# Optimization experiments

Hardware: AMD Instinct MI355X
Metric: run time of the kernel (lower is better)

The kernel has to match this reference:

```python
import jax, jax.numpy as jnp
import numpy as np

RES = 0.03
NUM_ROTS = 36
NUM_PROPOSAL = 256
OVERSAMPLE = 4           # fixed-size stand-in for the data-dependent while loop
GX, GY, GZ = 272, 112, 272  # grid covering [-4,4.16] x [-0.2,3.16] x [-4,4.16] at res=0.03
POW = 0.5
SEED_DIST_THRESH = 0.3


def setup_inputs() -> dict:
    key = jax.random.key(0)
    ks = jax.random.split(key, 6)
    N, M = 100000, 1024
    extent = jnp.array([7.0, 3.0, 7.0], jnp.float32)
    offset = jnp.array([-3.5, 0.0, -3.5], jnp.float32)
    pc = jax.random.uniform(ks[0], (N, 3), jnp.float32) * extent + offset
    xyz = jax.random.uniform(ks[1], (N, 3), jnp.float32, minval=-0.3, maxval=0.3)
    scale = jax.random.uniform(ks[2], (N, 3), jnp.float32, minval=0.1, maxval=1.0)
    prob = jax.random.uniform(ks[3], (N,), jnp.float32)
    corners = jnp.array([[-4.0, -0.2, -4.0], [4.16, 3.16, 4.16]], jnp.float32)
    vote_points = jax.random.uniform(ks[4], (M, 3), jnp.float32) * extent + offset
    return dict(pc=pc, xyz=xyz, scale=scale, prob=prob, corners=corners, vote_points=vote_points)


def hough_vote(pc, xyz, scale, prob, corners):
    # Each point casts NUM_ROTS votes: center = pc + R_y(theta) @ xyz_offset
    thetas = 2.0 * jnp.pi * jnp.arange(NUM_ROTS, dtype=jnp.float32) / NUM_ROTS
    c, s = jnp.cos(thetas), jnp.sin(thetas)  # [R]
    ox, oy, oz = xyz[:, 0:1], xyz[:, 1:2], xyz[:, 2:3]  # [N,1]
    rx = ox * c + oz * s      # [N,R]
    rz = -ox * s + oz * c     # [N,R]
    tx = pc[:, 0:1] + rx
    ty = jnp.broadcast_to(pc[:, 1:2] + oy, tx.shape)
    tz = pc[:, 2:3] + rz
    ix = jnp.floor((tx - corners[0, 0]) / RES + 0.5).astype(jnp.int32)
    iy = jnp.floor((ty - corners[0, 1]) / RES + 0.5).astype(jnp.int32)
    iz = jnp.floor((tz - corners[0, 2]) / RES + 0.5).astype(jnp.int32)
    inb = ((ix >= 0) & (ix < GX) & (iy >= 0) & (iy < GY) & (iz >= 0) & (iz < GZ))
    ixc = jnp.clip(ix, 0, GX - 1)
    iyc = jnp.clip(iy, 0, GY - 1)
    izc = jnp.clip(iz, 0, GZ - 1)
    flat = ((ixc * GY + iyc) * GZ + izc).ravel()  # [N*R]
    w = (prob[:, None] * inb.astype(prob.dtype))  # [N,R]
    grid_obj = jnp.zeros((GX * GY * GZ,), pc.dtype).at[flat].add(w.ravel())
    ws = (w[:, :, None] * scale[:, None, :]).reshape(-1, 3)
    grid_scale = jnp.zeros((GX * GY * GZ, 3), pc.dtype).at[flat].add(ws)
    hv_map = grid_obj.reshape(GX, GY, GZ)
    hv_scale = (grid_scale / (grid_obj[:, None] + 1e-7)).reshape(GX, GY, GZ, 3)
    return hv_map, hv_scale


def reference(pc, xyz, scale, prob, corners, vote_points):
    hv_map, hv_scale = hough_vote(pc, xyz, scale, prob, corners)
    hv_map_y = jnp.power(hv_map.max(axis=1) + 1e-7, POW)  # [GX,GZ]
    hv_map_yidx = jnp.argmax(hv_map, axis=1)              # [GX,GZ]
    dist = hv_map_y.reshape(-1)
    finite = jnp.isfinite(dist)
    safe = jnp.where(finite, dist, 0.0)
    ok = finite.all() & (safe.sum() >= 1e-7)
    dist = jnp.where(ok, safe, 1.0)

    # fixed-size oversampling instead of the data-dependent while loop
    K = NUM_PROPOSAL * OVERSAMPLE
    sample = jax.random.categorical(jax.random.key(42), jnp.log(dist + 1e-30), shape=(K,))
    sample_val = dist[sample]
    xi = sample // GZ
    zi = sample % GZ
    yi = hv_map_yidx[xi, zi]
    world_loc = jnp.stack([xi, yi, zi], -1).astype(pc.dtype) * RES + corners[0]  # [K,3]
    sc = hv_scale[xi, yi, zi, :]  # [K,3]

    # min distance to vote seeds; keep candidates near seeds (fallback: keep all)
    d2seed = jnp.min(jnp.linalg.norm(world_loc[:, None, :] - vote_points[None, :, :], axis=-1), axis=-1)
    keep = d2seed < SEED_DIST_THRESH
    keep = jnp.where(keep.any(), keep, jnp.ones_like(keep))
    order = jnp.argsort(jnp.where(keep, 0, 1))  # stable: passing candidates first
    sel = order[:NUM_PROPOSAL]
    candidates = world_loc[sel]
    scales_out = sc[sel]
    probs = jnp.zeros((NUM_PROPOSAL,), pc.dtype)
    return candidates, probs, scales_out
```

## Files before the change

kernel.cpp:

```cpp
#include <hip/hip_runtime.h>
#include <math.h>
#include <stdio.h>
#include <stdint.h>

#define GXD 272
#define GYD 112
#define GZD 272
#define NROT 36
#define CCLS (GXD*GZD)
#define KSMP 1024
#define NPROP 256
#define HSLOTS 2048
#define YH 56
#define NBINS (GXD*2)
#define SLICE (GYD*GZD)
#define SVCAP 64
#define ROWG 32

struct RotTab { float c[NROT]; float s[NROT]; };

__device__ __forceinline__ uint32_t cell_hash(int flat) {
    return ((uint32_t)flat * 2654435761u) >> 21;
}

#define ROTL_AB(x, r) __builtin_amdgcn_alignbit((x), (x), 32u - (r))

__device__ __forceinline__ uint32_t tf_bits(uint32_t i) {
    constexpr uint32_t K1  = 42u;
    constexpr uint32_t KS2 = 42u ^ 0x1BD11BDAu;
    uint32_t x0 = 0u, x1 = i + K1;
#define TF_R(r)  { x0 += x1; x1 = ROTL_AB(x1, r); x1 ^= x0; }
#define TF_RI(r, I0, I1) { x1 += (I1); x0 = x0 + (I0) + x1; x1 = ROTL_AB(x1, r); x1 ^= x0; }
    TF_R(13) TF_R(15) TF_R(26) TF_R(6)
    TF_RI(17, K1,  KS2 + 1u)  TF_R(29) TF_R(16) TF_R(24)
    TF_RI(13, KS2, 2u)        TF_R(15) TF_R(26) TF_R(6)
    TF_RI(17, 0u,  K1 + 3u)   TF_R(29) TF_R(16) TF_R(24)
    TF_RI(13, K1,  KS2 + 4u)  TF_R(15) TF_R(26) TF_R(6)
#undef TF_R
#undef TF_RI
    return (x0 + KS2) ^ (x1 + 5u);
}

__device__ __forceinline__ float uniform_from_bits(uint32_t b) {
    const float TINY = 1.1754943508222875e-38f;
    float f = __uint_as_float((b >> 9) | 0x3f800000u) - 1.0f;
    float u = __fadd_rn(__fmul_rn(f, 1.0f), TINY);
    return fmaxf(TINY, u);
}

__device__ __forceinline__ float gumbel_from_u(float u) {
    float l1 = (float)log((double)u);
    float l2 = (float)log((double)(-l1));
    return -l2;
}

__device__ __forceinline__ bool vote_iy(float py, float oy, float c0y, int& iy) {
    float ty = __fadd_rn(py, oy);
    float vy = __fadd_rn(__fdiv_rn(__fsub_rn(ty, c0y), 0.03f), 0.5f);
    iy = (int)floorf(vy);
    return (iy >= 0 && iy < GYD);
}
__device__ __forceinline__ bool vote_xz(float px, float pz, float ox, float oz,
                                        float c, float s, float c0x, float c0z,
                                        int& ix, int& iz) {
    float rx = __fadd_rn(__fmul_rn(ox, c), __fmul_rn(oz, s));
    float rz = __fadd_rn(__fmul_rn(-ox, s), __fmul_rn(oz, c));
    float tx = __fadd_rn(px, rx);
    float tz = __fadd_rn(pz, rz);
    float vx = __fadd_rn(__fdiv_rn(__fsub_rn(tx, c0x), 0.03f), 0.5f);
    float vz = __fadd_rn(__fdiv_rn(__fsub_rn(tz, c0z), 0.03f), 0.5f);
    ix = (int)floorf(vx);
    iz = (int)floorf(vz);
    return (ix >= 0 && ix < GXD && iz >= 0 && iz < GZD);
}

__global__ __launch_bounds__(256) void k_count(const float* __restrict__ pc, const float* __restrict__ xyz,
                          const float* __restrict__ corners, int N, RotTab rt,
                          int* __restrict__ bincnt, int* __restrict__ hblk) {
    __shared__ int h[NBINS];
    int tid = threadIdx.x;
    for (int j = tid; j < NBINS; j += 256) h[j] = 0;
    __syncthreads();
    int i = blockIdx.x * 256 + tid;
    if (i < N) {
        float px = pc[3*i], py = pc[3*i+1], pz = pc[3*i+2];
        float ox = xyz[3*i], oy = xyz[3*i+1], oz = xyz[3*i+2];
        int iy;
        if (vote_iy(py, oy, corners[1], iy)) {
            int ybit = (iy >= YH) ? 1 : 0;
            float c0x = corners[0], c0z = corners[2];
            for (int r = 0; r < NROT; ++r) {
                int ix, iz;
                if (vote_xz(px, pz, ox, oz, rt.c[r], rt.s[r], c0x, c0z, ix, iz))
                    atomicAdd(&h[ix*2 + ybit], 1);
            }
        }
    }
    __syncthreads();
    int* hb = hblk + (size_t)blockIdx.x * NBINS;
    for (int j = tid; j < NBINS; j += 256) {
        int cnt = h[j];
        hb[j] = cnt;
        if (cnt) atomicAdd(&bincnt[j], cnt);
    }
}

__global__ __launch_bounds__(576) void k_prefix(const int* __restrict__ bincnt,
                         int* __restrict__ binbase, int* __restrict__ bincur) {
    __shared__ int sc[576];
    int tid = threadIdx.x;
    int v = (tid < NBINS) ? bincnt[tid] : 0;
    sc[tid] = v;
    __syncthreads();
    for (int off = 1; off < 576; off <<= 1) {
        int x = sc[tid];
        if (tid >= off) x += sc[tid - off];
        __syncthreads();
        sc[tid] = x;
        __syncthreads();
    }
    if (tid < NBINS) {
        int excl = sc[tid] - v;
        binbase[tid] = excl;
        bincur[tid] = excl;
    }
}

__global__ __launch_bounds__(256) void k_binwrite(const float* __restrict__ pc, const float* __restrict__ xyz,
                          const float* __restrict__ prob, const float* __restrict__ corners,
                          int N, RotTab rt, int* __restrict__ bincur,
                          const int* __restrict__ hblk, uint2* __restrict__ vrec) {
    __shared__ int h[NBINS];
    __shared__ int bbase[NBINS];
    int tid = threadIdx.x;
    const int* hb = hblk + (size_t)blockIdx.x * NBINS;
    for (int j = tid; j < NBINS; j += 256) {
        int cnt = hb[j];
        bbase[j] = cnt ? atomicAdd(&bincur[j], cnt) : 0;
        h[j] = 0;
    }
    __syncthreads();
    int i = blockIdx.x * 256 + tid;
    if (i < N) {
        float px = pc[3*i], py = pc[3*i+1], pz = pc[3*i+2];
        float ox = xyz[3*i], oy = xyz[3*i+1], oz = xyz[3*i+2];
        int iy;
        if (vote_iy(py, oy, corners[1], iy)) {
            int ybit = (iy >= YH) ? 1 : 0;
            float c0x = corners[0], c0z = corners[2];
            float w0 = prob[i];
            for (int r = 0; r < NROT; ++r) {
                int ix, iz;
                if (vote_xz(px, pz, ox, oz, rt.c[r], rt.s[r], c0x, c0z, ix, iz)) {
                    int bin = ix*2 + ybit;
                    int rank = atomicAdd(&h[bin], 1);
                    int slot = bbase[bin] + rank;
                    vrec[slot] = make_uint2((uint32_t)((ix*GYD + iy)*GZD + iz), __float_as_uint(w0));
                }
            }
        }
    }
}

__global__ __launch_bounds__(256) void k_accum(const int* __restrict__ binbase,
                          const int* __restrict__ bincnt,
                          const uint2* __restrict__ vrec,
                          float* __restrict__ gobj,
                          unsigned long long* __restrict__ packed) {
    __shared__ float tile[YH*GZD];
    int b = blockIdx.x;
    int x = b >> 1, yh = b & 1;
    int tid = threadIdx.x;
    for (int j = tid; j < YH*GZD; j += 256) tile[j] = 0.0f;
    __syncthreads();
    int lo = binbase[b], n = bincnt[b];
    int xoff = x * SLICE;
    int yoff = yh * (YH*GZD);
    int sub = xoff + yoff;
    for (int j = lo + tid; j < lo + n; j += 256) {
        uint2 rec = vrec[j];
        atomicAdd(&tile[(int)rec.x - sub], __uint_as_float(rec.y));
    }
    __syncthreads();
    float* dst = gobj + (size_t)sub;
    for (int j = tid; j < YH*GZD; j += 256) dst[j] = tile[j];
    int ybase = yh * YH;
    for (int z = tid; z < GZD; z += 256) {
        float m = tile[z];
        int mi = 0;
        for (int y = 1; y < YH; ++y) {
            float v = tile[y*GZD + z];
            if (v > m) { m = v; mi = y; }
        }
        unsigned long long key = ((unsigned long long)__float_as_uint(m) << 32)
                               | (unsigned long long)(uint32_t)(0x7F - (ybase + mi));
        atomicMax(&packed[x*GZD + z], key);
    }
}

__global__ __launch_bounds__(256) void k_colmax2(const unsigned long long* __restrict__ packed,
                         float* __restrict__ logits, int* __restrict__ yidx,
                         float* __restrict__ sumdist) {
    int c = blockIdx.x * blockDim.x + threadIdx.x;
    unsigned long long key = packed[c];
    float m = __uint_as_float((uint32_t)(key >> 32));
    int mi = 0x7F - (int)(uint32_t)(key & 0xFFFFFFFFu);
    float d = __fsqrt_rn(__fadd_rn(m, 1e-7f));
    yidx[c] = mi;
    logits[c] = (float)log((double)__fadd_rn(d, 1e-30f));
    __shared__ float sred[256];
    int tid = threadIdx.x;
    sred[tid] = d; __syncthreads();
    for (int off = 128; off > 0; off >>= 1) {
        if (tid < off) sred[tid] += sred[tid+off];
        __syncthreads();
    }
    if (tid == 0) atomicAdd(sumdist, sred[0]);
}

__global__ __launch_bounds__(256) void k_thresh(const float* __restrict__ logits,
                                                const float* __restrict__ sumdist,
                                                uint32_t* __restrict__ bth) {
    int c = blockIdx.x * blockDim.x + threadIdx.x;
    if (c >= CCLS) return;
    double B0 = log((double)*sumdist) - 3.0;
    double t = exp(-exp((double)logits[c] - (B0 - 0.05)));
    long long k_th = (long long)floor(t * 8388608.0) - 2;
    uint32_t b;
    if (k_th <= 0)              b = 0u;
    else if (k_th >= 8388608LL) b = 0xFFFFFFFFu;
    else                        b = (uint32_t)k_th << 9;
    bth[c] = b;
}

__global__ __launch_bounds__(256) void k_prefilter(const uint32_t* __restrict__ bth,
                                                   int* __restrict__ svcnt,
                                                   uint2* __restrict__ svrec) {
    int c = blockIdx.x * 256 + threadIdx.x;
    int k0 = blockIdx.y * (KSMP / ROWG);
    uint32_t th = bth[c];
    uint32_t i = (uint32_t)k0 * (uint32_t)CCLS + (uint32_t)c;
#pragma unroll 4
    for (int kk = 0; kk < KSMP / ROWG; ++kk) {
        uint32_t bits = tf_bits(i);
        if (__builtin_expect(bits >= th, 0)) {
            int row = k0 + kk;
            int idx = atomicAdd(&svcnt[row], 1);
            if (idx < SVCAP) svrec[row * SVCAP + idx] = make_uint2((uint32_t)c, bits);
        }
        i += (uint32_t)CCLS;
    }
}

__global__ __launch_bounds__(64) void k_finalize(const float* __restrict__ logits,
                                                 const int* __restrict__ svcnt,
                                                 const uint2* __restrict__ svrec,
                                                 const int* __restrict__ yidx,
                                                 int* __restrict__ hkeys,
                                                 int* __restrict__ samples) {
    int k = blockIdx.x;
    int tid = threadIdx.x;
    int n = svcnt[k];
    float best = -INFINITY; int bc = 0x7fffffff;
    if (n > 0 && n <= SVCAP) {
        if (tid < n) {
            uint2 rec = svrec[k * SVCAP + tid];
            int c = (int)rec.x;
            best = __fadd_rn(gumbel_from_u(uniform_from_bits(rec.y)), logits[c]);
            bc = c;
        }
    } else {
        uint32_t base = (uint32_t)k * (uint32_t)CCLS;
        for (int c = tid; c < CCLS; c += 64) {
            float v = __fadd_rn(gumbel_from_u(uniform_from_bits(tf_bits(base + (uint32_t)c))), logits[c]);
            if (v > best || (v == best && c < bc)) { best = v; bc = c; }
        }
    }
    for (int off = 32; off > 0; off >>= 1) {
        float v2 = __shfl_down(best, off);
        int   i2 = __shfl_down(bc, off);
        if (v2 > best || (v2 == best && i2 < bc)) { best = v2; bc = i2; }
    }
    if (tid == 0) {
        samples[k] = bc;
        int xi = bc / GZD, zi = bc % GZD;
        int yi = yidx[bc];
        int flat = (xi*GYD + yi)*GZD + zi;
        uint32_t h = cell_hash(flat);
        for (;;) {
            int prev = atomicCAS(&hkeys[h], -1, flat);
            if (prev == -1 || prev == flat) break;
            h = (h + 1) & (HSLOTS - 1);
        }
    }
}

__global__ __launch_bounds__(256) void k_scale_scatter(const float* __restrict__ pc, const float* __restrict__ xyz,
                          const float* __restrict__ scale, const float* __restrict__ prob,
                          const float* __restrict__ corners,
                          const int* __restrict__ hkeys, float* __restrict__ gsmall,
                          int N, RotTab rt) {
    __shared__ int lk[HSLOTS];
    for (int j = threadIdx.x; j < HSLOTS; j += 256) lk[j] = hkeys[j];
    __syncthreads();
    int i = blockIdx.x * 256 + threadIdx.x;
    if (i >= N) return;
    float px = pc[3*i], py = pc[3*i+1], pz = pc[3*i+2];
    float ox = xyz[3*i], oy = xyz[3*i+1], oz = xyz[3*i+2];
    int iy;
    if (!vote_iy(py, oy, corners[1], iy)) return;
    float c0x = corners[0], c0z = corners[2];
    int iyo = iy * GZD;
    float w0 = prob[i];
    float ws0 = __fmul_rn(w0, scale[3*i]);
    float ws1 = __fmul_rn(w0, scale[3*i+1]);
    float ws2 = __fmul_rn(w0, scale[3*i+2]);
    for (int r = 0; r < NROT; ++r) {
        int ix, iz;
        if (!vote_xz(px, pz, ox, oz, rt.c[r], rt.s[r], c0x, c0z, ix, iz)) continue;
        int flat = ix * SLICE + iyo + iz;
        uint32_t h = cell_hash(flat);
        int slot = -1;
        for (;;) {
            int key = lk[h];
            if (key == flat) { slot = (int)h; break; }
            if (key == -1) break;
            h = (h + 1) & (HSLOTS - 1);
        }
        if (slot < 0) continue;
        atomicAdd(&gsmall[3*slot+0], ws0);
        atomicAdd(&gsmall[3*slot+1], ws1);
        atomicAdd(&gsmall[3*slot+2], ws2);
    }
}

__global__ __launch_bounds__(256) void k_post(const float* __restrict__ gobj,
                       const int* __restrict__ hkeys, const float* __restrict__ gsmall,
                       const int* __restrict__ yidx, const int* __restrict__ samples,
                       const float* __restrict__ corners, const float* __restrict__ vp, int M,
                       float* __restrict__ world, float* __restrict__ scv, int* __restrict__ keep) {
    int k = blockIdx.x;
    int tid = threadIdx.x;
    int s = samples[k];
    int xi = s / GZD, zi = s % GZD;
    int yi = yidx[s];
    float wx = __fadd_rn(__fmul_rn((float)xi, 0.03f), corners[0]);
    float wy = __fadd_rn(__fmul_rn((float)yi, 0.03f), corners[1]);
    float wz = __fadd_rn(__fmul_rn((float)zi, 0.03f), corners[2]);

    float dmin = INFINITY;
    for (int j = tid; j < M; j += 256) {
        float dx = __fsub_rn(wx, vp[3*j]);
        float dy = __fsub_rn(wy, vp[3*j+1]);
        float dz = __fsub_rn(wz, vp[3*j+2]);
        float sq = __fadd_rn(__fadd_rn(__fmul_rn(dx,dx), __fmul_rn(dy,dy)), __fmul_rn(dz,dz));
        dmin = fminf(dmin, __fsqrt_rn(sq));
    }
    __shared__ float sm[256];
    sm[tid] = dmin; __syncthreads();
    for (int off = 128; off > 0; off >>= 1) {
        if (tid < off) sm[tid] = fminf(sm[tid], sm[tid+off]);
        __syncthreads();
    }
    if (tid == 0) {
        world[3*k] = wx; world[3*k+1] = wy; world[3*k+2] = wz;
        int flat = (xi*GYD + yi)*GZD + zi;
        uint32_t h = cell_hash(flat);
        while (hkeys[h] != flat) h = (h + 1) & (HSLOTS - 1);
        float go = __fadd_rn(gobj[flat], 1e-7f);
        scv[3*k+0] = __fdiv_rn(gsmall[3*h+0], go);
        scv[3*k+1] = __fdiv_rn(gsmall[3*h+1], go);
        scv[3*k+2] = __fdiv_rn(gsmall[3*h+2], go);
        keep[k] = (sm[0] < 0.3f) ? 1 : 0;
    }
}

__global__ __launch_bounds__(256) void k_select(const float* __restrict__ world,
                                                const float* __restrict__ scv,
                                                const int* __restrict__ keep,
                                                float* __restrict__ out) {
    __shared__ int kp[KSMP];
    __shared__ int tsum[256];
    __shared__ int sel[NPROP];
    __shared__ int anyk;
    int tid = threadIdx.x;
    if (tid == 0) anyk = 0;
    __syncthreads();
    int a = 0;
    for (int j = tid; j < KSMP; j += 256) { int v = keep[j]; kp[j] = v; a |= v; }
    if (a) anyk = 1;
    __syncthreads();
    int any = anyk;
    int j0 = tid * 4;
    int k0v = any ? kp[j0]   : 1;
    int k1v = any ? kp[j0+1] : 1;
    int k2v = any ? kp[j0+2] : 1;
    int k3v = any ? kp[j0+3] : 1;
    int s0 = k0v, s1 = s0 + k1v, s2 = s1 + k2v, s3 = s2 + k3v;
    tsum[tid] = s3;
    __syncthreads();
    for (int off = 1; off < 256; off <<= 1) {
        int x = tsum[tid];
        if (tid >= off) x += tsum[tid - off];
        __syncthreads();
        tsum[tid] = x;
        __syncthreads();
    }
    int base = (tid > 0) ? tsum[tid-1] : 0;
    int nk = tsum[255];
    int inc[4] = { base + s0, base + s1, base + s2, base + s3 };
    int kv[4]  = { k0v, k1v, k2v, k3v };
    for (int q = 0; q < 4; ++q) {
        int j = j0 + q;
        int slot = kv[q] ? (inc[q] - 1) : (nk + j - inc[q]);
        if (slot < NPROP) sel[slot] = j;
    }
    __syncthreads();
    if (tid < NPROP) {
        int sidx = sel[tid];
        out[3*tid+0] = world[3*sidx+0];
        out[3*tid+1] = world[3*sidx+1];
        out[3*tid+2] = world[3*sidx+2];
        out[3*NPROP + tid] = 0.0f;
        out[4*NPROP + 3*tid + 0] = scv[3*sidx+0];
        out[4*NPROP + 3*tid + 1] = scv[3*sidx+1];
        out[4*NPROP + 3*tid + 2] = scv[3*sidx+2];
    }
}

extern "C" void kernel_launch(void* const* d_in, const int* in_sizes, int n_in,
                              void* d_out, int out_size, void* d_ws, size_t ws_size,
                              hipStream_t stream) {
    const float* pc      = (const float*)d_in[0];
    const float* xyz     = (const float*)d_in[1];
    const float* scale   = (const float*)d_in[2];
    const float* prob    = (const float*)d_in[3];
    const float* corners = (const float*)d_in[4];
    const float* vp      = (const float*)d_in[5];
    int N = in_sizes[0] / 3;
    int M = in_sizes[5] / 3;
    int NV = N * NROT;
    int pblocks = (N + 255) / 256;

    const size_t G = (size_t)GXD * GYD * GZD;
    float* gobj    = (float*)d_ws;
    float* sumdist = gobj + G;
    int*   bincnt  = (int*)(sumdist + 1);
    int*   svcnt   = bincnt + NBINS;
    unsigned long long* packed = (unsigned long long*)(svcnt + KSMP + 1);
    float* gsmall  = (float*)(packed + CCLS);
    size_t zero_bytes = (size_t)((char*)(gsmall + 3*HSLOTS) - (char*)sumdist);
    int*   binbase = (int*)(gsmall + 3*HSLOTS);
    int*   bincur  = binbase + NBINS;
    float* logits  = (float*)(bincur + NBINS);
    uint32_t* bth  = (uint32_t*)(logits + CCLS);
    int*   yidx    = (int*)(bth + CCLS);
    int*   samples = yidx + CCLS;
    int*   hkeys   = samples + KSMP;
    float* world   = (float*)(hkeys + HSLOTS);
    float* scv     = world + 3*KSMP;
    int*   keep    = (int*)(scv + 3*KSMP);
    uint2* svrec   = (uint2*)(((uintptr_t)(keep + KSMP) + 15) & ~(uintptr_t)15);
    int*   hblk    = (int*)(svrec + (size_t)KSMP * SVCAP);
    uint2* vrec    = (uint2*)(((uintptr_t)(hblk + (size_t)pblocks*NBINS) + 15) & ~(uintptr_t)15);
    size_t need = (size_t)((char*)(vrec + NV) - (char*)d_ws);
    if (ws_size < need) {
        fprintf(stderr, "kernel_launch: ws_size %zu < needed %zu\n", ws_size, need);
        return;
    }

    hipMemsetAsync(sumdist, 0, zero_bytes, stream);
    hipMemsetAsync(hkeys, 0xFF, HSLOTS*sizeof(int), stream);

    RotTab rt;
    const float twopi = (float)(2.0 * M_PI);
    for (int r = 0; r < NROT; ++r) {
        float th = (twopi * (float)r) / 36.0f;
        rt.c[r] = (float)cos((double)th);
        rt.s[r] = (float)sin((double)th);
    }

    k_count<<<pblocks, 256, 0, stream>>>(pc, xyz, corners, N, rt, bincnt, hblk);
    k_prefix<<<1, 576, 0, stream>>>(bincnt, binbase, bincur);
    k_binwrite<<<pblocks, 256, 0, stream>>>(pc, xyz, prob, corners, N, rt, bincur, hblk, vrec);
    k_accum<<<NBINS, 256, 0, stream>>>(binbase, bincnt, vrec, gobj, packed);
    k_colmax2<<<CCLS / 256, 256, 0, stream>>>(packed, logits, yidx, sumdist);
    k_thresh<<<CCLS / 256, 256, 0, stream>>>(logits, sumdist, bth);
    dim3 pf_grid(CCLS / 256, ROWG);
    k_prefilter<<<pf_grid, 256, 0, stream>>>(bth, svcnt, svrec);
    k_finalize<<<KSMP, 64, 0, stream>>>(logits, svcnt, svrec, yidx, hkeys, samples);
    k_scale_scatter<<<pblocks, 256, 0, stream>>>(pc, xyz, scale, prob, corners, hkeys, gsmall, N, rt);
    k_post<<<KSMP, 256, 0, stream>>>(gobj, hkeys, gsmall, yidx, samples, corners, vp, M, world, scv, keep);
    k_select<<<1, 256, 0, stream>>>(world, scv, keep, (float*)d_out);
}
```

Baseline: 393.5 us.

## Split Gumbel prefilter into data-independent speculative phase fused into earlier kernels

The categorical-sampling prefilter, which hashes all 1024x73984 random draws, now runs in two parts. The part that does not depend on the data tests a fixed high threshold and is spread as extra blocks across the count, binwrite, colmax and thresh launches, so it overlaps with the voting work. Cells whose per-cell threshold falls below that fixed threshold are written to a hot list, and a second-phase kernel rechecks only those cells for each sample row. Finalize now reduces over up to 96 records and checks its result against a bound, falling back to a full scan when the bound fails, which adds some risk in correctness and in load balance.

New measurement: 369.1 us. 1.07x faster.

```diff
diff --git a/kernel.cpp b/kernel.cpp
--- a/kernel.cpp
+++ b/kernel.cpp
@@ -8,14 +8,17 @@
 #define GZD 272
 #define NROT 36
 #define CCLS (GXD*GZD)
+#define CBLK (CCLS/256)
 #define KSMP 1024
 #define NPROP 256
 #define HSLOTS 2048
 #define YH 56
 #define NBINS (GXD*2)
 #define SLICE (GYD*GZD)
-#define SVCAP 64
-#define ROWG 32
+#define SVCAP 96
+#define AROWS 32
+#define AUNITS (CBLK * (KSMP/AROWS))
+#define TH_SPEC 0xFFE00000u
 
 struct RotTab { float c[NROT]; float s[NROT]; };
 
@@ -54,6 +57,25 @@
     return -l2;
 }
 
+__device__ __forceinline__ void phaseA_unit(int unit, int* __restrict__ svcnt,
+                                            uint2* __restrict__ svrec) {
+    int cb = unit % CBLK;
+    int rg = unit / CBLK;
+    int c  = cb * 256 + threadIdx.x;
+    int k0 = rg * AROWS;
+    uint32_t i = (uint32_t)k0 * (uint32_t)CCLS + (uint32_t)c;
+#pragma unroll 4
+    for (int kk = 0; kk < AROWS; ++kk) {
+        uint32_t bits = tf_bits(i);
+        if (__builtin_expect(bits >= TH_SPEC, 0)) {
+            int row = k0 + kk;
+            int idx = atomicAdd(&svcnt[row], 1);
+            if (idx < SVCAP) svrec[row * SVCAP + idx] = make_uint2((uint32_t)c, bits);
+        }
+        i += (uint32_t)CCLS;
+    }
+}
+
 __device__ __forceinline__ bool vote_iy(float py, float oy, float c0y, int& iy) {
     float ty = __fadd_rn(py, oy);
     float vy = __fadd_rn(__fdiv_rn(__fsub_rn(ty, c0y), 0.03f), 0.5f);
@@ -74,9 +96,11 @@
     return (ix >= 0 && ix < GXD && iz >= 0 && iz < GZD);
 }
 
-__global__ __launch_bounds__(256) void k_count(const float* __restrict__ pc, const float* __restrict__ xyz,
+__global__ __launch_bounds__(256) void k_count_b(const float* __restrict__ pc, const float* __restrict__ xyz,
                           const float* __restrict__ corners, int N, RotTab rt,
-                          int* __restrict__ bincnt, int* __restrict__ hblk) {
+                          int* __restrict__ bincnt, int* __restrict__ hblk,
+                          int nOrig, int unitBase, int* __restrict__ svcnt, uint2* __restrict__ svrec) {
+    if ((int)blockIdx.x >= nOrig) { phaseA_unit(unitBase + (int)blockIdx.x - nOrig, svcnt, svrec); return; }
     __shared__ int h[NBINS];
     int tid = threadIdx.x;
     for (int j = tid; j < NBINS; j += 256) h[j] = 0;
@@ -126,10 +150,12 @@
     }
 }
 
-__global__ __launch_bounds__(256) void k_binwrite(const float* __restrict__ pc, const float* __restrict__ xyz,
+__global__ __launch_bounds__(256) void k_binwrite_b(const float* __restrict__ pc, const float* __restrict__ xyz,
                           const float* __restrict__ prob, const float* __restrict__ corners,
                           int N, RotTab rt, int* __restrict__ bincur,
-                          const int* __restrict__ hblk, uint2* __restrict__ vrec) {
+                          const int* __restrict__ hblk, uint2* __restrict__ vrec,
+                          int nOrig, int unitBase, int* __restrict__ svcnt, uint2* __restrict__ svrec) {
+    if ((int)blockIdx.x >= nOrig) { phaseA_unit(unitBase + (int)blockIdx.x - nOrig, svcnt, svrec); return; }
     __shared__ int h[NBINS];
     __shared__ int bbase[NBINS];
     int tid = threadIdx.x;
@@ -198,10 +224,12 @@
     }
 }
 
-__global__ __launch_bounds__(256) void k_colmax2(const unsigned long long* __restrict__ packed,
+__global__ __launch_bounds__(256) void k_colmax2_b(const unsigned long long* __restrict__ packed,
                          float* __restrict__ logits, int* __restrict__ yidx,
-                         float* __restrict__ sumdist) {
-    int c = blockIdx.x * blockDim.x + threadIdx.x;
+                         float* __restrict__ sumdist,
+                         int nOrig, int unitBase, int* __restrict__ svcnt, uint2* __restrict__ svrec) {
+    if ((int)blockIdx.x >= nOrig) { phaseA_unit(unitBase + (int)blockIdx.x - nOrig, svcnt, svrec); return; }
+    int c = blockIdx.x * 256 + threadIdx.x;
     unsigned long long key = packed[c];
     float m = __uint_as_float((uint32_t)(key >> 32));
     int mi = 0x7F - (int)(uint32_t)(key & 0xFFFFFFFFu);
@@ -218,11 +246,14 @@
     if (tid == 0) atomicAdd(sumdist, sred[0]);
 }
 
-__global__ __launch_bounds__(256) void k_thresh(const float* __restrict__ logits,
-                                                const float* __restrict__ sumdist,
-                                                uint32_t* __restrict__ bth) {
-    int c = blockIdx.x * blockDim.x + threadIdx.x;
-    if (c >= CCLS) return;
+__global__ __launch_bounds__(256) void k_hotthresh_b(const float* __restrict__ logits,
+                                                     const float* __restrict__ sumdist,
+                                                     uint32_t* __restrict__ bth,
+                                                     int* __restrict__ hotcnt, int* __restrict__ hotlist,
+                                                     int nOrig, int unitBase,
+                                                     int* __restrict__ svcnt, uint2* __restrict__ svrec) {
+    if ((int)blockIdx.x >= nOrig) { phaseA_unit(unitBase + (int)blockIdx.x - nOrig, svcnt, svrec); return; }
+    int c = blockIdx.x * 256 + threadIdx.x;
     double B0 = log((double)*sumdist) - 3.0;
     double t = exp(-exp((double)logits[c] - (B0 - 0.05)));
     long long k_th = (long long)floor(t * 8388608.0) - 2;
@@ -231,28 +262,31 @@
     else if (k_th >= 8388608LL) b = 0xFFFFFFFFu;
     else                        b = (uint32_t)k_th << 9;
     bth[c] = b;
-}
-
-__global__ __launch_bounds__(256) void k_prefilter(const uint32_t* __restrict__ bth,
-                                                   int* __restrict__ svcnt,
-                                                   uint2* __restrict__ svrec) {
-    int c = blockIdx.x * 256 + threadIdx.x;
-    int k0 = blockIdx.y * (KSMP / ROWG);
-    uint32_t th = bth[c];
-    uint32_t i = (uint32_t)k0 * (uint32_t)CCLS + (uint32_t)c;
-#pragma unroll 4
-    for (int kk = 0; kk < KSMP / ROWG; ++kk) {
-        uint32_t bits = tf_bits(i);
-        if (__builtin_expect(bits >= th, 0)) {
-            int row = k0 + kk;
-            int idx = atomicAdd(&svcnt[row], 1);
-            if (idx < SVCAP) svrec[row * SVCAP + idx] = make_uint2((uint32_t)c, bits);
-        }
-        i += (uint32_t)CCLS;
+    if (b < TH_SPEC) {
+        int idx = atomicAdd(hotcnt, 1);
+        hotlist[idx] = c;
+    }
+}
+
+__global__ __launch_bounds__(256) void k_phaseB(const uint32_t* __restrict__ bth,
+                                                const int* __restrict__ hotlist,
+                                                const int* __restrict__ hotcnt,
+                                                int* __restrict__ svcnt, uint2* __restrict__ svrec) {
+    int k = blockIdx.x;
+    int n = *hotcnt;
+    uint32_t base = (uint32_t)k * (uint32_t)CCLS;
+    for (int j = threadIdx.x; j < n; j += 256) {
+        int c = hotlist[j];
+        uint32_t bits = tf_bits(base + (uint32_t)c);
+        if (bits >= bth[c] && bits < TH_SPEC) {
+            int idx = atomicAdd(&svcnt[k], 1);
+            if (idx < SVCAP) svrec[k * SVCAP + idx] = make_uint2((uint32_t)c, bits);
+        }
     }
 }
 
 __global__ __launch_bounds__(64) void k_finalize(const float* __restrict__ logits,
+                                                 const float* __restrict__ sumdist,
                                                  const int* __restrict__ svcnt,
                                                  const uint2* __restrict__ svrec,
                                                  const int* __restrict__ yidx,
@@ -262,24 +296,34 @@
     int tid = threadIdx.x;
     int n = svcnt[k];
     float best = -INFINITY; int bc = 0x7fffffff;
-    if (n > 0 && n <= SVCAP) {
-        if (tid < n) {
-            uint2 rec = svrec[k * SVCAP + tid];
+    bool full = (n <= 0 || n > SVCAP);
+    if (!full) {
+        for (int j = tid; j < n; j += 64) {
+            uint2 rec = svrec[k * SVCAP + j];
             int c = (int)rec.x;
-            best = __fadd_rn(gumbel_from_u(uniform_from_bits(rec.y)), logits[c]);
-            bc = c;
-        }
-    } else {
+            float v = __fadd_rn(gumbel_from_u(uniform_from_bits(rec.y)), logits[c]);
+            if (v > best || (v == best && c < bc)) { best = v; bc = c; }
+        }
+        for (int off = 32; off > 0; off >>= 1) {
+            float v2 = __shfl_xor(best, off);
+            int   i2 = __shfl_xor(bc, off);
+            if (v2 > best || (v2 == best && i2 < bc)) { best = v2; bc = i2; }
+        }
+        double B0 = log((double)*sumdist) - 3.0;
+        if (!((double)best > B0 - 0.05)) full = true;
+    }
+    if (full) {
+        best = -INFINITY; bc = 0x7fffffff;
         uint32_t base = (uint32_t)k * (uint32_t)CCLS;
         for (int c = tid; c < CCLS; c += 64) {
             float v = __fadd_rn(gumbel_from_u(uniform_from_bits(tf_bits(base + (uint32_t)c))), logits[c]);
             if (v > best || (v == best && c < bc)) { best = v; bc = c; }
         }
-    }
-    for (int off = 32; off > 0; off >>= 1) {
-        float v2 = __shfl_down(best, off);
-        int   i2 = __shfl_down(bc, off);
-        if (v2 > best || (v2 == best && i2 < bc)) { best = v2; bc = i2; }
+        for (int off = 32; off > 0; off >>= 1) {
+            float v2 = __shfl_xor(best, off);
+            int   i2 = __shfl_xor(bc, off);
+            if (v2 > best || (v2 == best && i2 < bc)) { best = v2; bc = i2; }
+        }
     }
     if (tid == 0) {
         samples[k] = bc;
@@ -447,7 +491,8 @@
     float* sumdist = gobj + G;
     int*   bincnt  = (int*)(sumdist + 1);
     int*   svcnt   = bincnt + NBINS;
-    unsigned long long* packed = (unsigned long long*)(svcnt + KSMP + 1);
+    int*   hotcnt  = svcnt + KSMP;
+    unsigned long long* packed = (unsigned long long*)(hotcnt + 1);
     float* gsmall  = (float*)(packed + CCLS);
     size_t zero_bytes = (size_t)((char*)(gsmall + 3*HSLOTS) - (char*)sumdist);
     int*   binbase = (int*)(gsmall + 3*HSLOTS);
@@ -461,7 +506,8 @@
     float* scv     = world + 3*KSMP;
     int*   keep    = (int*)(scv + 3*KSMP);
     uint2* svrec   = (uint2*)(((uintptr_t)(keep + KSMP) + 15) & ~(uintptr_t)15);
-    int*   hblk    = (int*)(svrec + (size_t)KSMP * SVCAP);
+    int*   hotlist = (int*)(svrec + (size_t)KSMP * SVCAP);
+    int*   hblk    = hotlist + CCLS;
     uint2* vrec    = (uint2*)(((uintptr_t)(hblk + (size_t)pblocks*NBINS) + 15) & ~(uintptr_t)15);
     size_t need = (size_t)((char*)(vrec + NV) - (char*)d_ws);
     if (ws_size < need) {
@@ -480,15 +526,20 @@
         rt.s[r] = (float)sin((double)th);
     }
 
-    k_count<<<pblocks, 256, 0, stream>>>(pc, xyz, corners, N, rt, bincnt, hblk);
+    const int BAL1 = 2800, BAL2 = 2800, BAL3 = 1900, BAL4 = AUNITS - BAL1 - BAL2 - BAL3;
+
+    k_count_b<<<pblocks + BAL1, 256, 0, stream>>>(pc, xyz, corners, N, rt, bincnt, hblk,
+                                                  pblocks, 0, svcnt, svrec);
     k_prefix<<<1, 576, 0, stream>>>(bincnt, binbase, bincur);
-    k_binwrite<<<pblocks, 256, 0, stream>>>(pc, xyz, prob, corners, N, rt, bincur, hblk, vrec);
+    k_binwrite_b<<<pblocks + BAL2, 256, 0, stream>>>(pc, xyz, prob, corners, N, rt, bincur, hblk, vrec,
+                                                     pblocks, BAL1, svcnt, svrec);
     k_accum<<<NBINS, 256, 0, stream>>>(binbase, bincnt, vrec, gobj, packed);
-    k_colmax2<<<CCLS / 256, 256, 0, stream>>>(packed, logits, yidx, sumdist);
-    k_thresh<<<CCLS / 256, 256, 0, stream>>>(logits, sumdist, bth);
-    dim3 pf_grid(CCLS / 256, ROWG);
-    k_prefilter<<<pf_grid, 256, 0, stream>>>(bth, svcnt, svrec);
-    k_finalize<<<KSMP, 64, 0, stream>>>(logits, svcnt, svrec, yidx, hkeys, samples);
+    k_colmax2_b<<<CBLK + BAL3, 256, 0, stream>>>(packed, logits, yidx, sumdist,
+                                                 CBLK, BAL1 + BAL2, svcnt, svrec);
+    k_hotthresh_b<<<CBLK + BAL4, 256, 0, stream>>>(logits, sumdist, bth, hotcnt, hotlist,
+                                                   CBLK, BAL1 + BAL2 + BAL3, svcnt, svrec);
+    k_phaseB<<<KSMP, 256, 0, stream>>>(bth, hotlist, hotcnt, svcnt, svrec);
+    k_finalize<<<KSMP, 64, 0, stream>>>(logits, sumdist, svcnt, svrec, yidx, hkeys, samples);
     k_scale_scatter<<<pblocks, 256, 0, stream>>>(pc, xyz, scale, prob, corners, hkeys, gsmall, N, rt);
     k_post<<<KSMP, 256, 0, stream>>>(gobj, hkeys, gsmall, yidx, samples, corners, vp, M, world, scv, keep);
     k_select<<<1, 256, 0, stream>>>(world, scv, keep, (float*)d_out);
```
